# Optimization experiments

Hardware: AMD Instinct MI355X
Metric: run time of the kernel (lower is better)

Reference implementation:

```python
import jax, jax.numpy as jnp
import numpy as np

PI = np.pi

def dct_2_1d(x):
    # DCT-II over last dim, norm=None, matching the torch FFT-based impl.
    N = x.shape[-1]
    v = jnp.concatenate([x[..., ::2], jnp.flip(x[..., 1::2], axis=-1)], axis=-1)
    Vc = jnp.fft.fft(v, axis=-1)
    k = -jnp.arange(N, dtype=x.dtype) * PI / (2 * N)
    V = Vc.real * jnp.cos(k) - Vc.imag * jnp.sin(k)
    return 2 * V

def idct_2_1d(X):
    # Inverse of dct_2_1d (scaled DCT-III), norm=None.
    N = X.shape[-1]
    X_v = X / 2
    k = jnp.arange(N, dtype=X.dtype) * PI / (2 * N)
    W_r, W_i = jnp.cos(k), jnp.sin(k)
    V_t_r = X_v
    V_t_i = jnp.concatenate([jnp.zeros_like(X_v[..., :1]), -jnp.flip(X_v, axis=-1)[..., :-1]], axis=-1)
    V_r = V_t_r * W_r - V_t_i * W_i
    V_i = V_t_r * W_i + V_t_i * W_r
    # torch.fft.irfft(complex, n=N) uses the first N//2+1 entries; numpy/jax irfft crops the same way.
    v = jnp.fft.irfft(V_r + 1j * V_i, n=N, axis=-1)
    x = jnp.zeros_like(v)
    x = x.at[..., ::2].set(v[..., :N - N // 2])
    x = x.at[..., 1::2].set(jnp.flip(v, axis=-1)[..., :N // 2])
    return x

def setup_inputs() -> dict:
    key = jax.random.key(0)
    k1, k2 = jax.random.split(key)
    B, N, C = 256, 196, 768  # N = h*w = 14*14, C = dim
    x = jax.random.normal(k1, (B, N, C), dtype=jnp.float32)
    weight = jax.random.normal(k2, (C, N), dtype=jnp.float32) * 0.02
    return {"x": x, "weight": weight}

def reference(x, weight):
    # x: [B, N, C]; weight: [C, N]
    xt = jnp.transpose(x, (0, 2, 1)).astype(jnp.float32)  # [B, C, N]
    X = dct_2_1d(xt)
    X = X * weight  # broadcast [C, N] over batch
    y = idct_2_1d(X)
    return jnp.transpose(y, (0, 2, 1))  # [B, N, C]
```

## Files before the change

### kernel.cpp

```cpp
#include <hip/hip_runtime.h>

typedef __bf16 bf16;
typedef __bf16 bf16x8 __attribute__((ext_vector_type(8)));
typedef __bf16 bf16x4 __attribute__((ext_vector_type(4)));
typedef float f32x4 __attribute__((ext_vector_type(4)));

#define N_DIM 196
#define C_DIM 768
#define B_DIM 256
#define KSTEPS 7
#define MT1 14
#define MT2 13
#define CT 64
#define LPITCH 232

#define D2F_ELEMS (MT1 * KSTEPS * 512)
#define EF_ELEMS  (MT2 * KSTEPS * 512)

__global__ void init_mats(bf16* __restrict__ d2f, bf16* __restrict__ ef) {
    int idx = blockIdx.x * 256 + threadIdx.x;
    const float PI = 3.14159265358979323846f;
    if (idx < D2F_ELEMS) {
        int j    = idx & 7;
        int lane = (idx >> 3) & 63;
        int rest = idx >> 9;
        int ks = rest % KSTEPS;
        int mt = rest / KSTEPS;
        int row = mt * 16 + (lane & 15);
        int col = ks * 32 + (lane >> 4) * 8 + j;
        float v = 0.0f;
        if (row < N_DIM && col < N_DIM) {
            int t = ((2 * col + 1) * row) % (4 * N_DIM);
            v = 2.0f * cosf(PI * (float)t / (float)(2 * N_DIM));
        }
        d2f[idx] = (bf16)v;
    } else {
        int e = idx - D2F_ELEMS;
        if (e < EF_ELEMS) {
            int j    = e & 7;
            int lane = (e >> 3) & 63;
            int rest = e >> 9;
            int ks = rest % KSTEPS;
            int mt = rest / KSTEPS;
            int row = mt * 16 + (lane & 15);
            int col = ks * 32 + (lane >> 4) * 8 + j;
            float v = 0.0f;
            if (row < N_DIM && col < N_DIM) {
                if (col == 0) {
                    v = 1.0f / (float)(2 * N_DIM);
                } else {
                    int t = ((2 * row + 1) * col) % (4 * N_DIM);
                    v = cosf(PI * (float)t / (float)(2 * N_DIM)) / (float)N_DIM;
                }
            }
            ef[e] = (bf16)v;
        }
    }
}

__global__ __launch_bounds__(256) void dct_fused(
        const float* __restrict__ x, const float* __restrict__ wgt,
        const bf16* __restrict__ d2f, const bf16* __restrict__ ef,
        float* __restrict__ out) {
    __shared__ bf16 lds[CT * LPITCH];

    const int b  = blockIdx.y;
    const int c0 = blockIdx.x * CT;
    const int t  = threadIdx.x;
    const int wave = t >> 6;
    const int lane = t & 63;
    const int ln15 = lane & 15;
    const int q    = lane >> 4;

    {
        int cj   = (t & 15) * 4;
        int mrow = t >> 4;
        for (int i = 0; i < MT1; ++i) {
            int m = i * 16 + mrow;
            float4 v = make_float4(0.f, 0.f, 0.f, 0.f);
            if (m < N_DIM)
                v = *(const float4*)(x + ((size_t)b * N_DIM + m) * C_DIM + c0 + cj);
            lds[(cj + 0) * LPITCH + m] = (bf16)v.x;
            lds[(cj + 1) * LPITCH + m] = (bf16)v.y;
            lds[(cj + 2) * LPITCH + m] = (bf16)v.z;
            lds[(cj + 3) * LPITCH + m] = (bf16)v.w;
        }
    }
    __syncthreads();

    f32x4 acc[4][4] = {};
    for (int ks = 0; ks < KSTEPS; ++ks) {
        bf16x8 bfr[4];
#pragma unroll
        for (int ct = 0; ct < 4; ++ct)
            bfr[ct] = *(const bf16x8*)(lds + (ct * 16 + ln15) * LPITCH + ks * 32 + q * 8);
#pragma unroll
        for (int ml = 0; ml < 4; ++ml) {
            int mt = wave + 4 * ml;
            if (mt < MT1) {
                bf16x8 afr = *(const bf16x8*)(d2f + ((size_t)(mt * KSTEPS + ks) * 64 + lane) * 8);
#pragma unroll
                for (int ct = 0; ct < 4; ++ct)
                    acc[ml][ct] = __builtin_amdgcn_mfma_f32_16x16x32_bf16(afr, bfr[ct], acc[ml][ct], 0, 0, 0);
            }
        }
    }
    __syncthreads();

#pragma unroll
    for (int ml = 0; ml < 4; ++ml) {
        int mt = wave + 4 * ml;
        if (mt >= MT1) continue;
        int kb = mt * 16 + q * 4;
#pragma unroll
        for (int ct = 0; ct < 4; ++ct) {
            int cc = ct * 16 + ln15;
            float4 wv = make_float4(0.f, 0.f, 0.f, 0.f);
            if (kb < N_DIM)
                wv = *(const float4*)(wgt + (size_t)(c0 + cc) * N_DIM + kb);
            bf16x4 pv;
            pv[0] = (bf16)(acc[ml][ct][0] * wv.x);
            pv[1] = (bf16)(acc[ml][ct][1] * wv.y);
            pv[2] = (bf16)(acc[ml][ct][2] * wv.z);
            pv[3] = (bf16)(acc[ml][ct][3] * wv.w);
            *(bf16x4*)(lds + cc * LPITCH + kb) = pv;
        }
    }
    __syncthreads();

    f32x4 acc2[4][4] = {};
    for (int ks = 0; ks < KSTEPS; ++ks) {
        bf16x8 bfr[4];
#pragma unroll
        for (int ct = 0; ct < 4; ++ct)
            bfr[ct] = *(const bf16x8*)(lds + (ct * 16 + ln15) * LPITCH + ks * 32 + q * 8);
#pragma unroll
        for (int ml = 0; ml < 4; ++ml) {
            int mt = wave + 4 * ml;
            if (mt < MT2) {
                bf16x8 afr = *(const bf16x8*)(ef + ((size_t)(mt * KSTEPS + ks) * 64 + lane) * 8);
#pragma unroll
                for (int ct = 0; ct < 4; ++ct)
                    acc2[ml][ct] = __builtin_amdgcn_mfma_f32_16x16x32_bf16(afr, bfr[ct], acc2[ml][ct], 0, 0, 0);
            }
        }
    }

#pragma unroll
    for (int ml = 0; ml < 4; ++ml) {
        int mt = wave + 4 * ml;
        if (mt >= MT2) continue;
#pragma unroll
        for (int ct = 0; ct < 4; ++ct) {
            int cc = ct * 16 + ln15;
#pragma unroll
            for (int r = 0; r < 4; ++r) {
                int n = mt * 16 + q * 4 + r;
                if (n < N_DIM)
                    out[((size_t)b * N_DIM + n) * C_DIM + c0 + cc] = acc2[ml][ct][r];
            }
        }
    }
}

extern "C" void kernel_launch(void* const* d_in, const int* in_sizes, int n_in,
                              void* d_out, int out_size, void* d_ws, size_t ws_size,
                              hipStream_t stream) {
    const float* x   = (const float*)d_in[0];
    const float* wgt = (const float*)d_in[1];
    float* out = (float*)d_out;

    bf16* d2f = (bf16*)d_ws;
    bf16* ef  = d2f + D2F_ELEMS;

    int tot = D2F_ELEMS + EF_ELEMS;
    init_mats<<<(tot + 255) / 256, 256, 0, stream>>>(d2f, ef);

    dim3 grid(C_DIM / CT, B_DIM);
    dct_fused<<<grid, 256, 0, stream>>>(x, wgt, d2f, ef, out);
}
```

Measured before the change: 342.4 us.

## Swizzle LDS layout, pre-permute weights into fragment order, vectorize transpose stores

The padded LDS pitch is replaced by a 256-wide XOR-swizzled layout meant to cut bank conflicts on the transposing writes and the fragment reads. The input load now reads four rows per thread and packs them into bf16x4 stores instead of scalar bf16 writes. The weight is re-laid out once per launch in the init kernel into MFMA accumulator order, so the scale step does one coalesced float4 load per fragment. A launch-bounds occupancy hint is also added, which may constrain register allocation.

```diff
diff --git a/kernel.cpp b/kernel.cpp
--- a/kernel.cpp
+++ b/kernel.cpp
@@ -12,12 +12,19 @@
 #define MT1 14
 #define MT2 13
 #define CT 64
-#define LPITCH 232
+#define NTILES 12
 
 #define D2F_ELEMS (MT1 * KSTEPS * 512)
 #define EF_ELEMS  (MT2 * KSTEPS * 512)
-
-__global__ void init_mats(bf16* __restrict__ d2f, bf16* __restrict__ ef) {
+#define WF_ELEMS  (NTILES * MT1 * 4 * 64 * 4)
+
+__device__ __forceinline__ int swz(int row, int off) {
+    return row * 256 + ((((off >> 3) ^ ((row >> 2) & 7) ^ ((row & 1) << 2)) << 3) | (off & 7));
+}
+
+__global__ void init_mats(const float* __restrict__ wgt,
+                          bf16* __restrict__ d2f, bf16* __restrict__ ef,
+                          float* __restrict__ wf) {
     int idx = blockIdx.x * 256 + threadIdx.x;
     const float PI = 3.14159265358979323846f;
     if (idx < D2F_ELEMS) {
@@ -34,38 +41,52 @@
             v = 2.0f * cosf(PI * (float)t / (float)(2 * N_DIM));
         }
         d2f[idx] = (bf16)v;
-    } else {
-        int e = idx - D2F_ELEMS;
-        if (e < EF_ELEMS) {
-            int j    = e & 7;
-            int lane = (e >> 3) & 63;
-            int rest = e >> 9;
-            int ks = rest % KSTEPS;
-            int mt = rest / KSTEPS;
-            int row = mt * 16 + (lane & 15);
-            int col = ks * 32 + (lane >> 4) * 8 + j;
-            float v = 0.0f;
-            if (row < N_DIM && col < N_DIM) {
-                if (col == 0) {
-                    v = 1.0f / (float)(2 * N_DIM);
-                } else {
-                    int t = ((2 * row + 1) * col) % (4 * N_DIM);
-                    v = cosf(PI * (float)t / (float)(2 * N_DIM)) / (float)N_DIM;
-                }
-            }
-            ef[e] = (bf16)v;
-        }
-    }
-}
-
-__global__ __launch_bounds__(256) void dct_fused(
-        const float* __restrict__ x, const float* __restrict__ wgt,
+        return;
+    }
+    idx -= D2F_ELEMS;
+    if (idx < EF_ELEMS) {
+        int j    = idx & 7;
+        int lane = (idx >> 3) & 63;
+        int rest = idx >> 9;
+        int ks = rest % KSTEPS;
+        int mt = rest / KSTEPS;
+        int row = mt * 16 + (lane & 15);
+        int col = ks * 32 + (lane >> 4) * 8 + j;
+        float v = 0.0f;
+        if (row < N_DIM && col < N_DIM) {
+            if (col == 0) v = 1.0f / (float)(2 * N_DIM);
+            else {
+                int t = ((2 * row + 1) * col) % (4 * N_DIM);
+                v = cosf(PI * (float)t / (float)(2 * N_DIM)) / (float)N_DIM;
+            }
+        }
+        ef[idx] = (bf16)v;
+        return;
+    }
+    idx -= EF_ELEMS;
+    if (idx < WF_ELEMS) {
+        int r    = idx & 3;
+        int lane = (idx >> 2) & 63;
+        int rest = idx >> 8;
+        int ct    = rest & 3;
+        int rest2 = rest >> 2;
+        int mt    = rest2 % MT1;
+        int ctile = rest2 / MT1;
+        int c = ctile * CT + ct * 16 + (lane & 15);
+        int k = mt * 16 + ((lane >> 4) & 3) * 4 + r;
+        wf[idx] = (k < N_DIM) ? wgt[(size_t)c * N_DIM + k] : 0.0f;
+    }
+}
+
+__global__ __launch_bounds__(256, 5) void dct_fused(
+        const float* __restrict__ x, const float* __restrict__ wf,
         const bf16* __restrict__ d2f, const bf16* __restrict__ ef,
         float* __restrict__ out) {
-    __shared__ bf16 lds[CT * LPITCH];
-
+    __shared__ bf16 lds[CT * 256];
+
+    const int ctile = blockIdx.x;
     const int b  = blockIdx.y;
-    const int c0 = blockIdx.x * CT;
+    const int c0 = ctile * CT;
     const int t  = threadIdx.x;
     const int wave = t >> 6;
     const int lane = t & 63;
@@ -73,17 +94,37 @@
     const int q    = lane >> 4;
 
     {
-        int cj   = (t & 15) * 4;
-        int mrow = t >> 4;
-        for (int i = 0; i < MT1; ++i) {
-            int m = i * 16 + mrow;
-            float4 v = make_float4(0.f, 0.f, 0.f, 0.f);
-            if (m < N_DIM)
-                v = *(const float4*)(x + ((size_t)b * N_DIM + m) * C_DIM + c0 + cj);
-            lds[(cj + 0) * LPITCH + m] = (bf16)v.x;
-            lds[(cj + 1) * LPITCH + m] = (bf16)v.y;
-            lds[(cj + 2) * LPITCH + m] = (bf16)v.z;
-            lds[(cj + 3) * LPITCH + m] = (bf16)v.w;
+        const int c4 = (t & 15) * 4;
+        const int mq = t >> 4;
+#pragma unroll
+        for (int i = 0; i < 4; ++i) {
+            int quad = i * 16 + mq;
+            if (quad > 55) continue;
+            int m0 = quad * 4;
+            float4 v0, v1, v2, v3;
+            if (quad <= 48) {
+                const float* p = x + ((size_t)b * N_DIM + m0) * C_DIM + c0 + c4;
+                v0 = *(const float4*)(p);
+                v1 = *(const float4*)(p + C_DIM);
+                v2 = *(const float4*)(p + 2 * C_DIM);
+                v3 = *(const float4*)(p + 3 * C_DIM);
+            } else {
+                v0 = v1 = v2 = v3 = make_float4(0.f, 0.f, 0.f, 0.f);
+            }
+            const float rx[4] = {v0.x, v1.x, v2.x, v3.x};
+            const float ry[4] = {v0.y, v1.y, v2.y, v3.y};
+            const float rz[4] = {v0.z, v1.z, v2.z, v3.z};
+            const float rw[4] = {v0.w, v1.w, v2.w, v3.w};
+            const float* rows[4] = {rx, ry, rz, rw};
+#pragma unroll
+            for (int k = 0; k < 4; ++k) {
+                bf16x4 pv;
+                pv[0] = (bf16)rows[k][0];
+                pv[1] = (bf16)rows[k][1];
+                pv[2] = (bf16)rows[k][2];
+                pv[3] = (bf16)rows[k][3];
+                *(bf16x4*)(lds + swz(c4 + k, m0)) = pv;
+            }
         }
     }
     __syncthreads();
@@ -93,7 +134,7 @@
         bf16x8 bfr[4];
 #pragma unroll
         for (int ct = 0; ct < 4; ++ct)
-            bfr[ct] = *(const bf16x8*)(lds + (ct * 16 + ln15) * LPITCH + ks * 32 + q * 8);
+            bfr[ct] = *(const bf16x8*)(lds + swz(ct * 16 + ln15, ks * 32 + q * 8));
 #pragma unroll
         for (int ml = 0; ml < 4; ++ml) {
             int mt = wave + 4 * ml;
@@ -115,15 +156,13 @@
 #pragma unroll
         for (int ct = 0; ct < 4; ++ct) {
             int cc = ct * 16 + ln15;
-            float4 wv = make_float4(0.f, 0.f, 0.f, 0.f);
-            if (kb < N_DIM)
-                wv = *(const float4*)(wgt + (size_t)(c0 + cc) * N_DIM + kb);
+            float4 wv = *(const float4*)(wf + ((size_t)((ctile * MT1 + mt) * 4 + ct) * 64 + lane) * 4);
             bf16x4 pv;
             pv[0] = (bf16)(acc[ml][ct][0] * wv.x);
             pv[1] = (bf16)(acc[ml][ct][1] * wv.y);
             pv[2] = (bf16)(acc[ml][ct][2] * wv.z);
             pv[3] = (bf16)(acc[ml][ct][3] * wv.w);
-            *(bf16x4*)(lds + cc * LPITCH + kb) = pv;
+            *(bf16x4*)(lds + swz(cc, kb)) = pv;
         }
     }
     __syncthreads();
@@ -133,7 +172,7 @@
         bf16x8 bfr[4];
 #pragma unroll
         for (int ct = 0; ct < 4; ++ct)
-            bfr[ct] = *(const bf16x8*)(lds + (ct * 16 + ln15) * LPITCH + ks * 32 + q * 8);
+            bfr[ct] = *(const bf16x8*)(lds + swz(ct * 16 + ln15, ks * 32 + q * 8));
 #pragma unroll
         for (int ml = 0; ml < 4; ++ml) {
             int mt = wave + 4 * ml;
@@ -170,12 +209,13 @@
     const float* wgt = (const float*)d_in[1];
     float* out = (float*)d_out;
 
-    bf16* d2f = (bf16*)d_ws;
-    bf16* ef  = d2f + D2F_ELEMS;
-
-    int tot = D2F_ELEMS + EF_ELEMS;
-    init_mats<<<(tot + 255) / 256, 256, 0, stream>>>(d2f, ef);
-
-    dim3 grid(C_DIM / CT, B_DIM);
-    dct_fused<<<grid, 256, 0, stream>>>(x, wgt, d2f, ef, out);
-}
+    bf16* d2f  = (bf16*)d_ws;
+    bf16* ef   = d2f + D2F_ELEMS;
+    float* wf  = (float*)(ef + EF_ELEMS);
+
+    int tot = D2F_ELEMS + EF_ELEMS + WF_ELEMS;
+    init_mats<<<(tot + 255) / 256, 256, 0, stream>>>(wgt, d2f, ef, wf);
+
+    dim3 grid(NTILES, B_DIM);
+    dct_fused<<<grid, 256, 0, stream>>>(x, wf, d2f, ef, out);
+}
```

Result: slower. 355.8 us (+3.9%).
